# Optimization experiments

Measured on AMD Instinct MI355X. Metric: run time of the kernel, lower is better.

The kernel has to match this reference:

```python
import jax, jax.numpy as jnp
import numpy as np
import math

B, C, H, W, D = 4, 64, 16, 16, 16
TEMB = 256
GROUPS = 16
EPS = 1e-5


def group_norm(x, gamma, beta, groups=GROUPS, eps=EPS):
    # x: [B, C, H, W, D]
    b, c, h, w, d = x.shape
    xg = x.reshape(b, groups, c // groups, h, w, d)
    mu = jnp.mean(xg, axis=(2, 3, 4, 5), keepdims=True)
    var = jnp.var(xg, axis=(2, 3, 4, 5), keepdims=True)
    xn = ((xg - mu) / jnp.sqrt(var + eps)).reshape(b, c, h, w, d)
    return xn * gamma[None, :, None, None, None] + beta[None, :, None, None, None]


def swish(x):
    return x * jax.nn.sigmoid(x)


def conv3d(x, w, b=None):
    y = jax.lax.conv_general_dilated(
        x, w, window_strides=(1, 1, 1), padding='SAME',
        dimension_numbers=('NCDHW', 'OIDHW', 'NCDHW'))
    if b is not None:
        y = y + b[None, :, None, None, None]
    return y


def setup_inputs() -> dict:
    key = jax.random.key(0)
    ks = jax.random.split(key, 16)
    s = lambda fan: 1.0 / math.sqrt(fan)
    inp = {
        'x': jax.random.normal(ks[0], (B, C, H, W, D), jnp.float32),
        'time_emb': jax.random.normal(ks[1], (B, TEMB), jnp.float32),
        # block1: GroupNorm + Conv3d(C->C, 3)
        'gn1_g': jnp.ones((C,), jnp.float32),
        'gn1_b': jnp.zeros((C,), jnp.float32),
        'conv1_w': jax.random.normal(ks[2], (C, C, 3, 3, 3), jnp.float32) * s(C * 27),
        'conv1_b': jnp.zeros((C,), jnp.float32),
        # time-embedding MLP: Linear(TEMB -> C)
        'mlp_w': jax.random.normal(ks[3], (C, TEMB), jnp.float32) * s(TEMB),
        'mlp_b': jnp.zeros((C,), jnp.float32),
        # block2: GroupNorm + Conv3d(C->C, 3)
        'gn2_g': jnp.ones((C,), jnp.float32),
        'gn2_b': jnp.zeros((C,), jnp.float32),
        'conv2_w': jax.random.normal(ks[4], (C, C, 3, 3, 3), jnp.float32) * s(C * 27),
        'conv2_b': jnp.zeros((C,), jnp.float32),
        # attention: GroupNorm, qkv 1x1 conv (no bias), out 1x1 conv
        'agn_g': jnp.ones((C,), jnp.float32),
        'agn_b': jnp.zeros((C,), jnp.float32),
        'qkv_w': jax.random.normal(ks[5], (3 * C, C), jnp.float32) * s(C),
        'out_w': jax.random.normal(ks[6], (C, C), jnp.float32) * s(C),
        'out_b': jnp.zeros((C,), jnp.float32),
    }
    return inp


def reference(x, time_emb, gn1_g, gn1_b, conv1_w, conv1_b, mlp_w, mlp_b,
              gn2_g, gn2_b, conv2_w, conv2_b, agn_g, agn_b, qkv_w, out_w, out_b):
    # --- ResnetBlock ---
    h = conv3d(swish(group_norm(x, gn1_g, gn1_b)), conv1_w, conv1_b)
    t = swish(time_emb) @ mlp_w.T + mlp_b                    # [B, C]
    h = h + t[:, :, None, None, None]
    h = conv3d(swish(group_norm(h, gn2_g, gn2_b)), conv2_w, conv2_b)
    x = h + x                                                # res_conv is Identity (dim == dim_out)
    # --- SelfAttention (n_head = 1) ---
    b, c, hh, ww, dd = x.shape
    n = hh * ww * dd
    norm = group_norm(x, agn_g, agn_b)
    qkv = jnp.einsum('oc,bchwd->bohwd', qkv_w, norm).reshape(b, 3 * c, n)
    q, k, v = jnp.split(qkv, 3, axis=1)                      # [B, C, N] each
    attn = jnp.einsum('bcn,bcm->bnm', q, k) / math.sqrt(c)   # [B, N, N]
    attn = jax.nn.softmax(attn, axis=-1)
    o = jnp.einsum('bnm,bcm->bcn', attn, v).reshape(b, c, hh, ww, dd)
    o = jnp.einsum('oc,bchwd->bohwd', out_w, o) + out_b[None, :, None, None, None]
    return o + x
```

## Files before the change

kernel.cpp:

```cpp
#include <hip/hip_runtime.h>
#include <math.h>

#define B 4
#define C 64
#define G 16
#define CPG 4
#define N 4096
#define TEMB 256

using f16x8 = __attribute__((ext_vector_type(8))) _Float16;
using f16x4 = __attribute__((ext_vector_type(4))) _Float16;
using f32x4 = __attribute__((ext_vector_type(4))) float;
using f32x16 = __attribute__((ext_vector_type(16))) float;
using h2 = __attribute__((ext_vector_type(2))) __fp16;

#define QSCALE 0.18033688f
#define SHIFT2 4.328085f

__device__ __forceinline__ int swzi(int row, int ci) {
  return (((ci >> 3) ^ (row & 7)) << 3) | (ci & 7);
}

__device__ __forceinline__ void gn_fin(const float2* pstats, const float* gamma,
                                       const float* beta, int b, int c,
                                       float& sc, float& sh) {
  int g = c >> 2;
  const float2* ps = pstats + ((size_t)(b * 16 + g)) * 4;
  float2 p0 = ps[0], p1 = ps[1], p2 = ps[2], p3 = ps[3];
  const float inv = 1.f / 16384.f;
  float mean = (p0.x + p1.x + p2.x + p3.x) * inv;
  float msq = (p0.y + p1.y + p2.y + p3.y) * inv;
  float var = msq - mean * mean;
  float rstd = rsqrtf(var + 1e-5f);
  sc = gamma[c] * rstd;
  sh = beta[c] - mean * sc;
}

__device__ __forceinline__ void gn_fin2(const float2* red, const float* gamma,
                                        const float* beta, int b, int c,
                                        float& sc, float& sh) {
  float2 r = red[b * 16 + (c >> 2)];
  const float inv = 1.f / 16384.f;
  float mean = r.x * inv;
  float var = r.y * inv - mean * mean;
  float rstd = rsqrtf(var + 1e-5f);
  sc = gamma[c] * rstd;
  sh = beta[c] - mean * sc;
}

__global__ void k_gnred(const float2* __restrict__ blkstats, float2* __restrict__ red) {
  int tid = threadIdx.x;
  int pair = tid >> 2, q = tid & 3;
  int b = pair >> 4, g = pair & 15;
  float sx = 0.f, sy = 0.f;
  for (int i = 0; i < 16; i++) {
    float2 v = blkstats[(size_t)(b * 64 + q * 16 + i) * 16 + g];
    sx += v.x; sy += v.y;
  }
  sx += __shfl_xor(sx, 1); sy += __shfl_xor(sy, 1);
  sx += __shfl_xor(sx, 2); sy += __shfl_xor(sy, 2);
  if (q == 0) { float2 r; r.x = sx; r.y = sy; red[pair] = r; }
}

__global__ void __launch_bounds__(256) k_prepgn(const float* __restrict__ w1,
                                                const float* __restrict__ w2,
                                                const float* __restrict__ temb,
                                                const float* __restrict__ mlp_w,
                                                const float* __restrict__ mlp_b,
                                                const float* __restrict__ x,
                                                _Float16* __restrict__ wf1,
                                                _Float16* __restrict__ wf2,
                                                float* __restrict__ tb,
                                                float2* __restrict__ pstats) {
  int bx = blockIdx.x, tid = threadIdx.x;
  __shared__ float sw[TEMB];
  __shared__ float part[4][64];
  __shared__ float ls[4], ls2[4];
  if (bx < 54) {
    const float* w = (bx < 27) ? w1 : w2;
    _Float16* wf = (bx < 27) ? wf1 : wf2;
    int tap = (bx < 27) ? bx : bx - 27;
    int co = tid >> 2, ci0 = (tid & 3) * 16;
    union { _Float16 hh[16]; f16x8 v[2]; } pk;
#pragma unroll
    for (int r = 0; r < 16; r++)
      pk.hh[r] = (_Float16)w[((size_t)(co * 64 + ci0 + r)) * 27 + tap];
    f16x8* dst = (f16x8*)(wf + ((size_t)tap * 64 + co) * 64 + ci0);
    dst[0] = pk.v[0]; dst[1] = pk.v[1];
  } else if (bx < 58) {
    int b = bx - 54;
    {
      float v = temb[b * TEMB + tid];
      sw[tid] = v / (1.f + __expf(-v));
    }
    __syncthreads();
    int co = tid & 63, seg = tid >> 6;
    float acc = 0.f;
#pragma unroll 16
    for (int k = 0; k < 64; k++) acc += sw[seg * 64 + k] * mlp_w[co * TEMB + seg * 64 + k];
    part[seg][co] = acc;
    __syncthreads();
    if (tid < 64) tb[b * C + tid] = part[0][tid] + part[1][tid] + part[2][tid] + part[3][tid] + mlp_b[tid];
  } else {
    int bx2 = bx - 58;
    const float4* xp = (const float4*)(x + (size_t)bx2 * 4096);
    float s = 0.f, s2 = 0.f;
#pragma unroll
    for (int kk = 0; kk < 4; kk++) {
      float4 v = xp[tid + kk * 256];
      s += v.x + v.y + v.z + v.w;
      s2 += v.x * v.x + v.y * v.y + v.z * v.z + v.w * v.w;
    }
#pragma unroll
    for (int off = 32; off > 0; off >>= 1) {
      s += __shfl_down(s, off);
      s2 += __shfl_down(s2, off);
    }
    int lane = tid & 63, wid = tid >> 6;
    if (lane == 0) { ls[wid] = s; ls2[wid] = s2; }
    __syncthreads();
    if (tid == 0) {
      float2 r;
      r.x = ls[0] + ls[1] + ls[2] + ls[3];
      r.y = ls2[0] + ls2[1] + ls2[2] + ls2[3];
      pstats[bx2] = r;
    }
  }
}

__global__ void __launch_bounds__(256) k_conv3f(const float* __restrict__ in,
                                                const float2* __restrict__ pstats,
                                                const float* __restrict__ gamma,
                                                const float* __restrict__ beta,
                                                const _Float16* __restrict__ wf,
                                                const float* __restrict__ bias,
                                                const float* __restrict__ addvec,
                                                const float* __restrict__ residual,
                                                float* __restrict__ out,
                                                float2* __restrict__ blkstats,
                                                int mode) {
  int bx = blockIdx.x;
  int b = bx >> 6, h = (bx >> 2) & 15, nog = bx & 3;
  int tid = threadIdx.x;
  int wv = tid >> 6, lane = tid & 63, hi = lane >> 5, l31 = lane & 31;
  int cw = wv >> 1, nw = wv & 1;
  __shared__ _Float16 a3[3][96][64];
  __shared__ _Float16 wl[2][64][64];
  __shared__ float2 scsh[64];
  __shared__ float2 sg[16];
  if (tid < 64) {
    float sc, sh;
    if (mode == 0) gn_fin(pstats, gamma, beta, b, tid, sc, sh);
    else gn_fin2(pstats, gamma, beta, b, tid, sc, sh);
    float2 r; r.x = sc; r.y = sh;
    scsh[tid] = r;
  }
  if (tid >= 64 && tid < 80) { sg[tid - 64].x = 0.f; sg[tid - 64].y = 0.f; }
  __syncthreads();
  int w0 = nog * 4 - 1;
  for (int i = tid; i < 2304; i += 256) {
    int r = i / 768, rem = i % 768;
    int ci8 = rem / 96, ns = rem % 96;
    int wp = w0 + (ns >> 4), dd = ns & 15;
    int hin = h + r - 1;
    f16x8 val = {};
    if ((unsigned)hin < 16u && (unsigned)wp < 16u) {
      const float* src = in + (((size_t)(b * 64 + ci8 * 8) * 16 + hin) * 256) + wp * 16 + dd;
      union { _Float16 hh[8]; f16x8 v; } pk;
#pragma unroll
      for (int j = 0; j < 8; j++) {
        float v = src[(size_t)j * 4096];
        float2 ss = scsh[ci8 * 8 + j];
        float t = v * ss.x + ss.y;
        pk.hh[j] = (_Float16)(t / (1.f + __expf(-t)));
      }
      val = pk.v;
    }
    *(f16x8*)&a3[r][ns][swzi(ns, ci8 * 8)] = val;
  }
#pragma unroll
  for (int q = 0; q < 2; q++) {
    int chunk = tid + q * 256;
    int co = chunk >> 3, ci8 = chunk & 7;
    f16x8 v = *(const f16x8*)(wf + (size_t)co * 64 + ci8 * 8);
    *(f16x8*)&wl[0][co][swzi(co, ci8 * 8)] = v;
  }
  f32x16 acc = {};
  __syncthreads();
  int cur = 0;
  int co_r = cw * 32 + l31;
  int n_loc = nw * 32 + l31;
  int wrow = n_loc >> 4;
  int d = n_loc & 15;
  for (int t = 0; t < 27; t++) {
    f16x8 pw0 = {}, pw1 = {};
    if (t < 26) {
      pw0 = *(const f16x8*)(wf + ((size_t)(t + 1) * 64 + (tid >> 3)) * 64 + (tid & 7) * 8);
      pw1 = *(const f16x8*)(wf + ((size_t)(t + 1) * 64 + ((tid + 256) >> 3)) * 64 + (tid & 7) * 8);
    }
    int kw = (t / 3) % 3, kd = t % 3, kh = t / 9;
    int wpl = wrow + kw;
    int dp = d + kd - 1;
    bool ok = (unsigned)dp < 16u;
    int ns = wpl * 16 + dp;
#pragma unroll
    for (int c4 = 0; c4 < 4; c4++) {
      int ci = c4 * 16 + hi * 8;
      f16x8 af = *(const f16x8*)&wl[cur][co_r][swzi(co_r, ci)];
      f16x8 bf = {};
      if (ok) bf = *(const f16x8*)&a3[kh][ns][swzi(ns, ci)];
      acc = __builtin_amdgcn_mfma_f32_32x32x16_f16(af, bf, acc, 0, 0, 0);
    }
    if (t < 26) {
      *(f16x8*)&wl[cur ^ 1][tid >> 3][swzi(tid >> 3, (tid & 7) * 8)] = pw0;
      *(f16x8*)&wl[cur ^ 1][(tid + 256) >> 3][swzi((tid + 256) >> 3, (tid & 7) * 8)] = pw1;
      __syncthreads();
      cur ^= 1;
    }
  }
  int nq = nog * 64 + n_loc;
  float gs[4] = {0.f, 0.f, 0.f, 0.f}, gs2[4] = {0.f, 0.f, 0.f, 0.f};
#pragma unroll
  for (int r = 0; r < 16; r++) {
    int co = cw * 32 + (r & 3) + 8 * (r >> 2) + 4 * hi;
    size_t off = (((size_t)(b * 64 + co)) * 16 + h) * 256 + nq;
    float vv = acc[r] + bias[co] + (addvec ? addvec[b * 64 + co] : 0.f);
    if (residual) vv += residual[off];
    out[off] = vv;
    gs[r >> 2] += vv;
    gs2[r >> 2] += vv * vv;
  }
#pragma unroll
  for (int off2 = 1; off2 < 32; off2 <<= 1)
#pragma unroll
    for (int rq = 0; rq < 4; rq++) {
      gs[rq] += __shfl_xor(gs[rq], off2);
      gs2[rq] += __shfl_xor(gs2[rq], off2);
    }
  if (l31 == 0) {
#pragma unroll
    for (int rq = 0; rq < 4; rq++) {
      int g = cw * 8 + 2 * rq + hi;
      atomicAdd(&sg[g].x, gs[rq]);
      atomicAdd(&sg[g].y, gs2[rq]);
    }
  }
  __syncthreads();
  if (tid < 16) blkstats[(size_t)bx * 16 + tid] = sg[tid];
}

__global__ void __launch_bounds__(256) k_qkv(const float* __restrict__ x2,
                                             const float2* __restrict__ red,
                                             const float* __restrict__ gamma,
                                             const float* __restrict__ beta,
                                             const float* __restrict__ w,
                                             _Float16* __restrict__ qh, _Float16* __restrict__ kh,
                                             _Float16* __restrict__ vh) {
  int b = blockIdx.x >> 6, nt = blockIdx.x & 63;
  int n0 = nt * 64;
  __shared__ __align__(16) float xl[64][64];
  __shared__ float wl[192 * 64];
  int tid = threadIdx.x;
  for (int i = tid; i < 192 * 64; i += 256) wl[i] = w[i];
  {
    int c = tid >> 2, seg = tid & 3;
    float sc, sh;
    gn_fin2(red, gamma, beta, b, c, sc, sh);
    const float4* src = (const float4*)(x2 + ((size_t)(b * C + c)) * N + n0);
    float4* dst = (float4*)&xl[c][seg * 16];
#pragma unroll
    for (int j = 0; j < 4; j++) {
      float4 v = src[seg * 4 + j];
      v.x = v.x * sc + sh; v.y = v.y * sc + sh; v.z = v.z * sc + sh; v.w = v.w * sc + sh;
      dst[j] = v;
    }
  }
  __syncthreads();
  int nq = tid & 15, og = tid >> 4;
  float4 acc[12];
#pragma unroll
  for (int j = 0; j < 12; j++) acc[j] = make_float4(0.f, 0.f, 0.f, 0.f);
  for (int c = 0; c < 64; c++) {
    float4 xv = *(const float4*)&xl[c][nq * 4];
#pragma unroll
    for (int j = 0; j < 12; j++) {
      float wv = wl[(og * 12 + j) * 64 + c];
      acc[j].x += wv * xv.x; acc[j].y += wv * xv.y; acc[j].z += wv * xv.z; acc[j].w += wv * xv.w;
    }
  }
#pragma unroll
  for (int j = 0; j < 12; j++) {
    int o3 = og * 12 + j;
    if (o3 >= 128) {
      f16x4 pv;
      pv[0] = (_Float16)acc[j].x; pv[1] = (_Float16)acc[j].y;
      pv[2] = (_Float16)acc[j].z; pv[3] = (_Float16)acc[j].w;
      int c = o3 - 128;
      int t = (n0 >> 4) + (nq >> 2);
      *(f16x4*)(vh + ((size_t)(b * 256 + t) * 64 + c) * 16 + (nq & 3) * 4) = pv;
    }
  }
  __syncthreads();
#pragma unroll
  for (int j = 0; j < 12; j++) {
    int o3 = og * 12 + j;
    if (o3 < 64) {
      float4 v = acc[j];
      v.x *= QSCALE; v.y *= QSCALE; v.z *= QSCALE; v.w *= QSCALE;
      *(float4*)&xl[o3][nq * 4] = v;
    }
  }
  __syncthreads();
  {
    int n_ = tid >> 2, cs = (tid & 3) * 16;
    union { _Float16 hh[16]; uint4 u[2]; } pk;
#pragma unroll
    for (int r = 0; r < 16; r++) pk.hh[r] = (_Float16)xl[cs + r][n_];
    uint4* dst = (uint4*)(qh + ((size_t)b * N + n0 + n_) * 64 + cs);
    dst[0] = pk.u[0]; dst[1] = pk.u[1];
  }
  __syncthreads();
#pragma unroll
  for (int j = 0; j < 12; j++) {
    int o3 = og * 12 + j;
    if (o3 >= 64 && o3 < 128) *(float4*)&xl[o3 - 64][nq * 4] = acc[j];
  }
  __syncthreads();
  {
    int n_ = tid >> 2, cs = (tid & 3) * 16;
    union { _Float16 hh[16]; uint4 u[2]; } pk;
#pragma unroll
    for (int r = 0; r < 16; r++) pk.hh[r] = (_Float16)xl[cs + r][n_];
    uint4* dst = (uint4*)(kh + ((size_t)b * N + n0 + n_) * 64 + cs);
    dst[0] = pk.u[0]; dst[1] = pk.u[1];
  }
}

__global__ void __launch_bounds__(256) k_attn(const _Float16* __restrict__ q,
                                              const _Float16* __restrict__ k,
                                              const _Float16* __restrict__ v,
                                              _Float16* __restrict__ po,
                                              float* __restrict__ pl) {
  int bx = blockIdx.x;
  int xcd = bx & 7, i6 = bx >> 3;
  int nt = i6 & 63, phi = i6 >> 6;
  int p = phi * 8 + xcd;
  int s = p >> 2, b = p & 3;
  int n0 = nt * 64;
  int tid = threadIdx.x;
  int wv = tid >> 6, lane = tid & 63, lg = lane >> 4, ll = lane & 15;
  __shared__ float ol[64][72];
  __shared__ float lsum[4][64];
  const _Float16* qp = q + (size_t)b * N * 64;
  f16x8 qf[4][2];
#pragma unroll
  for (int qb = 0; qb < 4; qb++)
#pragma unroll
    for (int ch = 0; ch < 2; ch++)
      qf[qb][ch] = *(const f16x8*)(qp + (size_t)(n0 + qb * 16 + ll) * 64 + ch * 32 + lg * 8);
  f32x4 oacc[4][4] = {};
  f32x4 lfrag[4] = {};
  const f16x4 ones = {(_Float16)1.f, (_Float16)1.f, (_Float16)1.f, (_Float16)1.f};
  const _Float16* kptr = k + (size_t)b * N * 64 + (size_t)(s * 1024 + wv * 16 + ll) * 64 + lg * 8;
  const _Float16* vptr = v + ((size_t)(b * 256 + s * 64 + wv) * 64 + ll) * 16 + lg * 4;
  f16x8 kf0 = *(const f16x8*)(kptr);
  f16x8 kf1 = *(const f16x8*)(kptr + 32);
  f16x4 vf[4];
#pragma unroll
  for (int cb = 0; cb < 4; cb++) vf[cb] = *(const f16x4*)(vptr + cb * 256);
  for (int it = 0; it < 16; it++) {
    const _Float16* kptrn = kptr + 4096;
    const _Float16* vptrn = vptr + 4096;
    f32x4 sv[4];
    __builtin_amdgcn_s_setprio(1);
#pragma unroll
    for (int qb = 0; qb < 4; qb++) {
      f32x4 z = {-SHIFT2, -SHIFT2, -SHIFT2, -SHIFT2};
      z = __builtin_amdgcn_mfma_f32_16x16x32_f16(kf0, qf[qb][0], z, 0, 0, 0);
      sv[qb] = __builtin_amdgcn_mfma_f32_16x16x32_f16(kf1, qf[qb][1], z, 0, 0, 0);
    }
    __builtin_amdgcn_s_setprio(0);
    f16x8 nk0 = *(const f16x8*)(kptrn);
    f16x8 nk1 = *(const f16x8*)(kptrn + 32);
    f16x4 nv[4];
#pragma unroll
    for (int cb = 0; cb < 4; cb++) nv[cb] = *(const f16x4*)(vptrn + cb * 256);
    f16x4 pk[4];
#pragma unroll
    for (int qb = 0; qb < 4; qb++) {
      float e0 = __builtin_amdgcn_exp2f(sv[qb][0]);
      float e1 = __builtin_amdgcn_exp2f(sv[qb][1]);
      float e2 = __builtin_amdgcn_exp2f(sv[qb][2]);
      float e3 = __builtin_amdgcn_exp2f(sv[qb][3]);
      union { h2 h[2]; f16x4 v4; } u;
      u.h[0] = __builtin_amdgcn_cvt_pkrtz(e0, e1);
      u.h[1] = __builtin_amdgcn_cvt_pkrtz(e2, e3);
      pk[qb] = u.v4;
    }
    __builtin_amdgcn_s_setprio(1);
#pragma unroll
    for (int qb = 0; qb < 4; qb++) {
#pragma unroll
      for (int cb = 0; cb < 4; cb++)
        oacc[qb][cb] = __builtin_amdgcn_mfma_f32_16x16x16f16(vf[cb], pk[qb], oacc[qb][cb], 0, 0, 0);
      lfrag[qb] = __builtin_amdgcn_mfma_f32_16x16x16f16(ones, pk[qb], lfrag[qb], 0, 0, 0);
    }
    __builtin_amdgcn_s_setprio(0);
    kf0 = nk0; kf1 = nk1;
#pragma unroll
    for (int cb = 0; cb < 4; cb++) vf[cb] = nv[cb];
    kptr = kptrn; vptr = vptrn;
  }
  if (lane < 16) {
#pragma unroll
    for (int qb = 0; qb < 4; qb++) lsum[wv][qb * 16 + lane] = lfrag[qb][0];
  }
  for (int w = 0; w < 4; w++) {
    __syncthreads();
    if (wv == w) {
#pragma unroll
      for (int qb = 0; qb < 4; qb++)
#pragma unroll
        for (int cb = 0; cb < 4; cb++) {
          float* a = &ol[qb * 16 + ll][cb * 16 + 4 * lg];
          if (w == 0) {
            *(f32x4*)a = oacc[qb][cb];
          } else {
            f32x4 t = *(f32x4*)a;
            t += oacc[qb][cb];
            *(f32x4*)a = t;
          }
        }
    }
  }
  __syncthreads();
  {
    int n = tid >> 2, cq = (tid & 3) * 16;
    float lt = lsum[0][n] + lsum[1][n] + lsum[2][n] + lsum[3][n];
    float inv = 1.f / lt;
    union { _Float16 hh[16]; uint4 u[2]; } pk2;
#pragma unroll
    for (int j = 0; j < 16; j++) pk2.hh[j] = (_Float16)(ol[n][cq + j] * inv);
    uint4* dst = (uint4*)(po + ((size_t)(s * 4 + b) * N + n0 + n) * 64 + cq);
    dst[0] = pk2.u[0]; dst[1] = pk2.u[1];
    if (tid < 64)
      pl[(size_t)(s * 4 + b) * N + n0 + tid] =
          lsum[0][tid] + lsum[1][tid] + lsum[2][tid] + lsum[3][tid];
  }
}

__global__ void __launch_bounds__(256) k_outproj(const _Float16* __restrict__ po,
                                                 const float* __restrict__ pl,
                                                 const float* __restrict__ w,
                                                 const float* __restrict__ bias,
                                                 const float* __restrict__ x2,
                                                 float* __restrict__ out) {
  int b = blockIdx.x >> 6, nt = blockIdx.x & 63;
  int n0 = nt * 64;
  __shared__ __align__(16) float wl2[64][68];
  __shared__ __align__(16) float ol[64][68];
  __shared__ float wsc[4][64];
  int tid = threadIdx.x;
  if (tid < 64) {
    float l0 = pl[((size_t)(0 * 4 + b)) * N + n0 + tid];
    float l1 = pl[((size_t)(1 * 4 + b)) * N + n0 + tid];
    float l2 = pl[((size_t)(2 * 4 + b)) * N + n0 + tid];
    float l3 = pl[((size_t)(3 * 4 + b)) * N + n0 + tid];
    float inv = 1.f / (l0 + l1 + l2 + l3);
    wsc[0][tid] = l0 * inv; wsc[1][tid] = l1 * inv;
    wsc[2][tid] = l2 * inv; wsc[3][tid] = l3 * inv;
  }
  for (int i = tid; i < 4096; i += 256) wl2[i >> 6][i & 63] = w[i];
  __syncthreads();
  for (int base = tid; base < 1024; base += 256) {
    int n = base >> 4, c0 = (base & 15) * 4;
    float a0 = 0.f, a1 = 0.f, a2 = 0.f, a3 = 0.f;
#pragma unroll
    for (int s = 0; s < 4; s++) {
      f16x4 pv = *(const f16x4*)&po[((size_t)(s * 4 + b) * N + n0 + n) * 64 + c0];
      float wsv = wsc[s][n];
      a0 += (float)pv[0] * wsv; a1 += (float)pv[1] * wsv;
      a2 += (float)pv[2] * wsv; a3 += (float)pv[3] * wsv;
    }
    ol[n][c0] = a0; ol[n][c0 + 1] = a1; ol[n][c0 + 2] = a2; ol[n][c0 + 3] = a3;
  }
  __syncthreads();
  int co = tid & 63, ng = tid >> 6;
  float acc16[16];
#pragma unroll
  for (int i = 0; i < 16; i++) acc16[i] = 0.f;
  for (int c4 = 0; c4 < 16; c4++) {
    float4 wv = *(const float4*)&wl2[co][c4 * 4];
#pragma unroll
    for (int i = 0; i < 16; i++) {
      float4 ov = *(const float4*)&ol[ng * 16 + i][c4 * 4];
      acc16[i] += wv.x * ov.x + wv.y * ov.y + wv.z * ov.z + wv.w * ov.w;
    }
  }
  float bv = bias[co];
  __syncthreads();
#pragma unroll
  for (int i = 0; i < 16; i++) ol[ng * 16 + i][co] = acc16[i] + bv;
  __syncthreads();
  for (int kk = 0; kk < 16; kk++) {
    int i = tid + kk * 256;
    int c2 = i >> 6, nl = i & 63;
    size_t idx = ((size_t)(b * C + c2)) * N + n0 + nl;
    out[idx] = ol[nl][c2] + x2[idx];
  }
}

extern "C" void kernel_launch(void* const* d_in, const int* in_sizes, int n_in,
                              void* d_out, int out_size, void* d_ws, size_t ws_size,
                              hipStream_t stream) {
  (void)in_sizes; (void)n_in; (void)out_size; (void)ws_size;
  const float* x       = (const float*)d_in[0];
  const float* temb    = (const float*)d_in[1];
  const float* gn1_g   = (const float*)d_in[2];
  const float* gn1_b   = (const float*)d_in[3];
  const float* conv1_w = (const float*)d_in[4];
  const float* conv1_b = (const float*)d_in[5];
  const float* mlp_w   = (const float*)d_in[6];
  const float* mlp_b   = (const float*)d_in[7];
  const float* gn2_g   = (const float*)d_in[8];
  const float* gn2_b   = (const float*)d_in[9];
  const float* conv2_w = (const float*)d_in[10];
  const float* conv2_b = (const float*)d_in[11];
  const float* agn_g   = (const float*)d_in[12];
  const float* agn_b   = (const float*)d_in[13];
  const float* qkv_w   = (const float*)d_in[14];
  const float* out_w   = (const float*)d_in[15];
  const float* out_b   = (const float*)d_in[16];
  float* out = (float*)d_out;
  float* ws = (float*)d_ws;
  const size_t F = 1048576;
  float* h        = ws;
  float* x2       = ws + F;
  _Float16* qh    = (_Float16*)(ws + 2 * F);
  _Float16* khb   = qh + F;
  _Float16* vhb   = khb + F;
  float2* pst1 = (float2*)(vhb + F);
  float* tb    = (float*)(pst1 + 256);
  _Float16* wf1 = (_Float16*)(tb + 256);
  _Float16* wf2 = wf1 + 27 * 64 * 64;
  _Float16* po  = wf2 + 27 * 64 * 64;
  float* pl     = (float*)(po + 4 * F);
  float2* pstb1 = (float2*)(pl + 65536);
  float2* pstb2 = pstb1 + 4096;
  float2* red2  = pstb2 + 4096;
  float2* red3  = red2 + 64;

  k_prepgn<<<314, 256, 0, stream>>>(conv1_w, conv2_w, temb, mlp_w, mlp_b, x,
                                    wf1, wf2, tb, pst1);
  k_conv3f<<<256, 256, 0, stream>>>(x, pst1, gn1_g, gn1_b, wf1, conv1_b, tb, nullptr,
                                    h, pstb1, 0);
  k_gnred<<<1, 256, 0, stream>>>(pstb1, red2);
  k_conv3f<<<256, 256, 0, stream>>>(h, (const float2*)red2, gn2_g, gn2_b, wf2, conv2_b,
                                    nullptr, x, x2, pstb2, 1);
  k_gnred<<<1, 256, 0, stream>>>(pstb2, red3);
  k_qkv<<<256, 256, 0, stream>>>(x2, (const float2*)red3, agn_g, agn_b, qkv_w, qh, khb, vhb);
  k_attn<<<1024, 256, 0, stream>>>(qh, khb, vhb, po, pl);
  k_outproj<<<256, 256, 0, stream>>>(po, pl, out_w, out_b, x2, out);
}
```

Before: 119.1 us.

## Store conv inputs in fp16 and fold group-norm reductions into consumers

The two k_gnred launches are removed. Each consumer kernel (second conv, qkv) now sums the 64 per-block partial stats itself for every channel. The input x is also written as fp16 during the stats pass, and conv1's output is stored in fp16, which halves the bytes read by the gather loops in both convs. This saves two tiny launches and some memory traffic. In exchange, each block does redundant stats sums, and the intermediate h loses precision because it is stored in fp16 before group norm.

```diff
diff --git a/kernel.cpp b/kernel.cpp
--- a/kernel.cpp
+++ b/kernel.cpp
@@ -36,30 +36,23 @@
   sh = beta[c] - mean * sc;
 }
 
-__device__ __forceinline__ void gn_fin2(const float2* red, const float* gamma,
-                                        const float* beta, int b, int c,
-                                        float& sc, float& sh) {
-  float2 r = red[b * 16 + (c >> 2)];
+__device__ __forceinline__ void gn_fin_blk(const float2* blk, const float* gamma,
+                                           const float* beta, int b, int c,
+                                           float& sc, float& sh) {
+  int g = c >> 2;
+  float sx = 0.f, sy = 0.f;
+  const float2* p = blk + (size_t)(b * 64) * 16 + g;
+#pragma unroll 8
+  for (int i = 0; i < 64; i++) {
+    float2 v = p[(size_t)i * 16];
+    sx += v.x; sy += v.y;
+  }
   const float inv = 1.f / 16384.f;
-  float mean = r.x * inv;
-  float var = r.y * inv - mean * mean;
+  float mean = sx * inv;
+  float var = sy * inv - mean * mean;
   float rstd = rsqrtf(var + 1e-5f);
   sc = gamma[c] * rstd;
   sh = beta[c] - mean * sc;
-}
-
-__global__ void k_gnred(const float2* __restrict__ blkstats, float2* __restrict__ red) {
-  int tid = threadIdx.x;
-  int pair = tid >> 2, q = tid & 3;
-  int b = pair >> 4, g = pair & 15;
-  float sx = 0.f, sy = 0.f;
-  for (int i = 0; i < 16; i++) {
-    float2 v = blkstats[(size_t)(b * 64 + q * 16 + i) * 16 + g];
-    sx += v.x; sy += v.y;
-  }
-  sx += __shfl_xor(sx, 1); sy += __shfl_xor(sy, 1);
-  sx += __shfl_xor(sx, 2); sy += __shfl_xor(sy, 2);
-  if (q == 0) { float2 r; r.x = sx; r.y = sy; red[pair] = r; }
 }
 
 __global__ void __launch_bounds__(256) k_prepgn(const float* __restrict__ w1,
@@ -71,7 +64,8 @@
                                                 _Float16* __restrict__ wf1,
                                                 _Float16* __restrict__ wf2,
                                                 float* __restrict__ tb,
-                                                float2* __restrict__ pstats) {
+                                                float2* __restrict__ pstats,
+                                                _Float16* __restrict__ xh) {
   int bx = blockIdx.x, tid = threadIdx.x;
   __shared__ float sw[TEMB];
   __shared__ float part[4][64];
@@ -104,12 +98,17 @@
   } else {
     int bx2 = bx - 58;
     const float4* xp = (const float4*)(x + (size_t)bx2 * 4096);
+    f16x4* xhp = (f16x4*)xh + (size_t)bx2 * 1024;
     float s = 0.f, s2 = 0.f;
 #pragma unroll
     for (int kk = 0; kk < 4; kk++) {
       float4 v = xp[tid + kk * 256];
       s += v.x + v.y + v.z + v.w;
       s2 += v.x * v.x + v.y * v.y + v.z * v.z + v.w * v.w;
+      f16x4 hv;
+      hv[0] = (_Float16)v.x; hv[1] = (_Float16)v.y;
+      hv[2] = (_Float16)v.z; hv[3] = (_Float16)v.w;
+      xhp[tid + kk * 256] = hv;
     }
 #pragma unroll
     for (int off = 32; off > 0; off >>= 1) {
@@ -128,15 +127,17 @@
   }
 }
 
-__global__ void __launch_bounds__(256) k_conv3f(const float* __restrict__ in,
+__global__ void __launch_bounds__(256) k_conv3f(const _Float16* __restrict__ in,
                                                 const float2* __restrict__ pstats,
+                                                const float2* __restrict__ prevblk,
                                                 const float* __restrict__ gamma,
                                                 const float* __restrict__ beta,
                                                 const _Float16* __restrict__ wf,
                                                 const float* __restrict__ bias,
                                                 const float* __restrict__ addvec,
                                                 const float* __restrict__ residual,
-                                                float* __restrict__ out,
+                                                _Float16* __restrict__ outh,
+                                                float* __restrict__ outf,
                                                 float2* __restrict__ blkstats,
                                                 int mode) {
   int bx = blockIdx.x;
@@ -151,7 +152,7 @@
   if (tid < 64) {
     float sc, sh;
     if (mode == 0) gn_fin(pstats, gamma, beta, b, tid, sc, sh);
-    else gn_fin2(pstats, gamma, beta, b, tid, sc, sh);
+    else gn_fin_blk(prevblk, gamma, beta, b, tid, sc, sh);
     float2 r; r.x = sc; r.y = sh;
     scsh[tid] = r;
   }
@@ -165,11 +166,11 @@
     int hin = h + r - 1;
     f16x8 val = {};
     if ((unsigned)hin < 16u && (unsigned)wp < 16u) {
-      const float* src = in + (((size_t)(b * 64 + ci8 * 8) * 16 + hin) * 256) + wp * 16 + dd;
+      const _Float16* src = in + (((size_t)(b * 64 + ci8 * 8) * 16 + hin) * 256) + wp * 16 + dd;
       union { _Float16 hh[8]; f16x8 v; } pk;
 #pragma unroll
       for (int j = 0; j < 8; j++) {
-        float v = src[(size_t)j * 4096];
+        float v = (float)src[(size_t)j * 4096];
         float2 ss = scsh[ci8 * 8 + j];
         float t = v * ss.x + ss.y;
         pk.hh[j] = (_Float16)(t / (1.f + __expf(-t)));
@@ -225,8 +226,12 @@
     int co = cw * 32 + (r & 3) + 8 * (r >> 2) + 4 * hi;
     size_t off = (((size_t)(b * 64 + co)) * 16 + h) * 256 + nq;
     float vv = acc[r] + bias[co] + (addvec ? addvec[b * 64 + co] : 0.f);
-    if (residual) vv += residual[off];
-    out[off] = vv;
+    if (mode == 1) {
+      vv += residual[off];
+      outf[off] = vv;
+    } else {
+      outh[off] = (_Float16)vv;
+    }
     gs[r >> 2] += vv;
     gs2[r >> 2] += vv * vv;
   }
@@ -250,7 +255,7 @@
 }
 
 __global__ void __launch_bounds__(256) k_qkv(const float* __restrict__ x2,
-                                             const float2* __restrict__ red,
+                                             const float2* __restrict__ prevblk,
                                              const float* __restrict__ gamma,
                                              const float* __restrict__ beta,
                                              const float* __restrict__ w,
@@ -260,18 +265,26 @@
   int n0 = nt * 64;
   __shared__ __align__(16) float xl[64][64];
   __shared__ float wl[192 * 64];
+  __shared__ float2 scsh[64];
   int tid = threadIdx.x;
+  if (tid < 64) {
+    float sc, sh;
+    gn_fin_blk(prevblk, gamma, beta, b, tid, sc, sh);
+    float2 r; r.x = sc; r.y = sh;
+    scsh[tid] = r;
+  }
   for (int i = tid; i < 192 * 64; i += 256) wl[i] = w[i];
+  __syncthreads();
   {
     int c = tid >> 2, seg = tid & 3;
-    float sc, sh;
-    gn_fin2(red, gamma, beta, b, c, sc, sh);
+    float2 ss = scsh[c];
     const float4* src = (const float4*)(x2 + ((size_t)(b * C + c)) * N + n0);
     float4* dst = (float4*)&xl[c][seg * 16];
 #pragma unroll
     for (int j = 0; j < 4; j++) {
       float4 v = src[seg * 4 + j];
-      v.x = v.x * sc + sh; v.y = v.y * sc + sh; v.z = v.z * sc + sh; v.w = v.w * sc + sh;
+      v.x = v.x * ss.x + ss.y; v.y = v.y * ss.x + ss.y;
+      v.z = v.z * ss.x + ss.y; v.w = v.w * ss.x + ss.y;
       dst[j] = v;
     }
   }
@@ -534,9 +547,10 @@
   float* out = (float*)d_out;
   float* ws = (float*)d_ws;
   const size_t F = 1048576;
-  float* h        = ws;
-  float* x2       = ws + F;
-  _Float16* qh    = (_Float16*)(ws + 2 * F);
+  float* x2       = ws;
+  _Float16* xh    = (_Float16*)(ws + F);
+  _Float16* hbuf  = xh + F;
+  _Float16* qh    = hbuf + F;
   _Float16* khb   = qh + F;
   _Float16* vhb   = khb + F;
   float2* pst1 = (float2*)(vhb + F);
@@ -547,18 +561,14 @@
   float* pl     = (float*)(po + 4 * F);
   float2* pstb1 = (float2*)(pl + 65536);
   float2* pstb2 = pstb1 + 4096;
-  float2* red2  = pstb2 + 4096;
-  float2* red3  = red2 + 64;
 
   k_prepgn<<<314, 256, 0, stream>>>(conv1_w, conv2_w, temb, mlp_w, mlp_b, x,
-                                    wf1, wf2, tb, pst1);
-  k_conv3f<<<256, 256, 0, stream>>>(x, pst1, gn1_g, gn1_b, wf1, conv1_b, tb, nullptr,
-                                    h, pstb1, 0);
-  k_gnred<<<1, 256, 0, stream>>>(pstb1, red2);
-  k_conv3f<<<256, 256, 0, stream>>>(h, (const float2*)red2, gn2_g, gn2_b, wf2, conv2_b,
-                                    nullptr, x, x2, pstb2, 1);
-  k_gnred<<<1, 256, 0, stream>>>(pstb2, red3);
-  k_qkv<<<256, 256, 0, stream>>>(x2, (const float2*)red3, agn_g, agn_b, qkv_w, qh, khb, vhb);
+                                    wf1, wf2, tb, pst1, xh);
+  k_conv3f<<<256, 256, 0, stream>>>(xh, pst1, nullptr, gn1_g, gn1_b, wf1, conv1_b,
+                                    tb, nullptr, hbuf, nullptr, pstb1, 0);
+  k_conv3f<<<256, 256, 0, stream>>>(hbuf, nullptr, pstb1, gn2_g, gn2_b, wf2, conv2_b,
+                                    nullptr, x, nullptr, x2, pstb2, 1);
+  k_qkv<<<256, 256, 0, stream>>>(x2, pstb2, agn_g, agn_b, qkv_w, qh, khb, vhb);
   k_attn<<<1024, 256, 0, stream>>>(qh, khb, vhb, po, pl);
   k_outproj<<<256, 256, 0, stream>>>(po, pl, out_w, out_b, x2, out);
 }
```

After: 117.3 us, median of 2. No clear change (-1.5%).
